# Kernel tuning notes

Hardware: AMD Instinct MI355X
Metric: run time of the kernel (lower is better)

## Reference

```python
import jax, jax.numpy as jnp
import numpy as np

SIZE = 96          # input layer neurons per side
SIZE_NEXT = 96     # first diffractive layer neurons per side
LENGTH = 1e-3      # physical aperture length (m)
Z0 = 0.0           # z of input layer
Z1 = 1e-2          # z of first diffractive layer
WAVELENGTH = 1.55e-6
TWO_PI = jnp.float32(2.0 * np.pi)


def _coords(n_size, n_length, z):
    # matrix[i, j] = ((i+0.5)*dl, (j+0.5)*dl, z), dl = n_length/n_size; flattened row-major
    idx = (jnp.arange(n_size, dtype=jnp.float32) + 0.5) * (n_length / n_size)
    x = jnp.repeat(idx, n_size)   # varies with first index
    y = jnp.tile(idx, n_size)     # varies with second index
    return x, y, jnp.float32(z)


def setup_inputs() -> dict:
    key = jax.random.key(0)
    x = jax.random.uniform(key, (SIZE, SIZE), dtype=jnp.float32)
    return {"x": x}


def reference(x):
    sx, sy, sz = _coords(SIZE, LENGTH, Z0)            # sources: (S2,)
    dx, dy, dz_plane = _coords(SIZE_NEXT, LENGTH, Z1)  # detectors: (D2,)
    # normalize image to unit amplitude, phase 0 (complex weights)
    weights = (x / jnp.max(x)).reshape(-1).astype(jnp.complex64)  # (S2,)
    # all-pairs distances (D2, S2); z separation is a scalar constant
    ddx = dx[:, None] - sx[None, :]
    ddy = dy[:, None] - sy[None, :]
    dz = dz_plane - sz
    r = jnp.sqrt(ddx * ddx + ddy * ddy + dz * dz)
    # Rayleigh-Sommerfeld secondary-source term: w = (z/r^2) * (1/(2*pi*r) + 1/(j*lambda)) * exp(j*2*pi*r/lambda)
    inv_jlam = jnp.complex64(1.0 / (1j * WAVELENGTH))
    amp = (dz / (r * r)) * ((1.0 / (TWO_PI * r)).astype(jnp.complex64) + inv_jlam)
    w = amp * jnp.exp(1j * ((TWO_PI / WAVELENGTH) * r))  # complex64 (D2, S2)
    modes = (w @ weights).reshape(SIZE_NEXT, SIZE_NEXT)
    return modes
```

## Files before the change

kernel.cpp:

```cpp
#include <hip/hip_runtime.h>

namespace rs7 {

constexpr int kN   = 96;
constexpr int kN2  = kN * kN;
constexpr int kDetPerBlock = 256;
constexpr int kSiPerBlock  = 6;
constexpr int kDetBlocks   = kN2 / kDetPerBlock;
constexpr int kSiSplits    = kN / kSiPerBlock;
constexpr int kGrid  = kDetBlocks * kSiSplits;
constexpr int kBlock = 256;
constexpr int kMaxRows = 9;
constexpr int kCols    = 2 * kN - 1;

__global__ __launch_bounds__(kBlock) void rs_table_v7(const float* __restrict__ img,
                                                      float* __restrict__ out) {
    const float dl      = (float)(1e-3 / 96.0);
    const float dz      = 0.01f;
    const float dz2     = dz * dz;
    const float lam_amp = (float)(1.0 / 1.55e-6);
    const float inv_2pi = 1.0f / 6.2831855f;
    const float k32     = 6.2831855f / 1.55e-6f;

    __shared__ float2 tab[kMaxRows * kCols];
    __shared__ float  wts[kSiPerBlock * kN];
    __shared__ float  smax[4];

    const int tid  = (int)threadIdx.x;
    const int lane = tid & 63;
    const int wid  = tid >> 6;

    const int db = (int)blockIdx.x >> 4;
    const int ss = (int)blockIdx.x & 15;
    const int d0 = db * kDetPerBlock;
    const int di_lo = d0 / kN;
    const int di_hi = (d0 + kDetPerBlock - 1) / kN;
    const int si_lo = ss * kSiPerBlock;
    const int si_hi = si_lo + kSiPerBlock - 1;

    int amin;
    if (di_lo <= si_hi && si_lo <= di_hi) amin = 0;
    else amin = (di_lo > si_hi) ? (di_lo - si_hi) : (si_lo - di_hi);
    const int amax  = max(di_hi - si_lo, si_hi - di_lo);
    const int nrows = amax - amin + 1;

    for (int e = tid; e < nrows * kCols; e += kBlock) {
        const int ra = e / kCols;
        const int c  = e - ra * kCols;
        const float ax = (float)(amin + ra) * dl;
        const float by = (float)(c - (kN - 1)) * dl;
        const float r  = sqrtf(ax * ax + by * by + dz2);
        const float theta = k32 * r;
        float sn, cs;
        __sincosf(theta, &sn, &cs);
        sn = sinf(theta);
        cs = cosf(theta);
        const float rinv = 1.0f / r;
        const float ampf = dz * rinv * rinv;
        const float near = rinv * inv_2pi;
        float2 wv;
        wv.x = ampf * (near * cs + lam_amp * sn);
        wv.y = ampf * (near * sn - lam_amp * cs);
        tab[e] = wv;
    }

    for (int t = tid; t < kSiPerBlock * kN; t += kBlock) {
        wts[t] = img[si_lo * kN + t];
    }

    float vmax = 0.0f;
    for (int t = tid; t < kN2; t += kBlock) vmax = fmaxf(vmax, img[t]);
    for (int off = 32; off >= 1; off >>= 1) vmax = fmaxf(vmax, __shfl_xor(vmax, off, 64));
    if (lane == 0) smax[wid] = vmax;
    __syncthreads();
    const float inv_max = 1.0f / fmaxf(fmaxf(smax[0], smax[1]), fmaxf(smax[2], smax[3]));

    const int det = d0 + wid * 64 + lane;
    const int di  = det / kN;
    const int dj  = det - di * kN;

    float acc_re = 0.0f, acc_im = 0.0f;

    for (int sl = 0; sl < kSiPerBlock; ++sl) {
        const int si = si_lo + sl;
        int av = di - si;
        if (av < 0) av = -av;
        const float2* __restrict__ rowp = tab + (av - amin) * kCols + dj;
        const float*  __restrict__ wrow = wts + sl * kN;
#pragma unroll
        for (int sj = 0; sj < kN; ++sj) {
            const float2 wv  = rowp[(kN - 1) - sj];
            const float  wgt = wrow[sj];
            acc_re = fmaf(wv.x, wgt, acc_re);
            acc_im = fmaf(wv.y, wgt, acc_im);
        }
    }

    atomicAdd(&out[det],       acc_re * inv_max);
    atomicAdd(&out[kN2 + det], acc_im * inv_max);
}

}

extern "C" void kernel_launch(void* const* d_in, const int* in_sizes, int n_in,
                              void* d_out, int out_size, void* d_ws, size_t ws_size,
                              hipStream_t stream) {
    (void)in_sizes; (void)n_in; (void)d_ws; (void)ws_size;
    const float* img = (const float*)d_in[0];
    float* out = (float*)d_out;
    hipMemsetAsync(d_out, 0, (size_t)out_size * sizeof(float), stream);
    hipLaunchKernelGGL(rs7::rs_table_v7, dim3(rs7::kGrid), dim3(rs7::kBlock),
                       0, stream, img, out);
}
```

Measured before the change: 76.64 us.

## Split into fp16-table conv kernel plus separate split-reduction kernel

Stores the precomputed Green's-function table in shared memory as scaled fp16 pairs instead of float2, halving LDS traffic, and reads image weights directly from global memory. Each block now covers 4 source rows instead of 6, which gives more blocks. Partial sums go to a workspace slab per split, with no atomics and no memset. A second kernel computes the max normalization once per block and sums the splits. This risks precision loss from fp16 table entries and adds a second launch plus workspace traffic.

Result: faster. 70.70 us (-7.7%).

```diff
diff --git a/kernel.cpp b/kernel.cpp
--- a/kernel.cpp
+++ b/kernel.cpp
@@ -1,20 +1,25 @@
 #include <hip/hip_runtime.h>
 
-namespace rs7 {
+namespace rs8 {
 
-constexpr int kN   = 96;
-constexpr int kN2  = kN * kN;
+constexpr int kN    = 96;
+constexpr int kN2   = kN * kN;
+constexpr int kOut2 = 2 * kN2;
 constexpr int kDetPerBlock = 256;
-constexpr int kSiPerBlock  = 6;
 constexpr int kDetBlocks   = kN2 / kDetPerBlock;
-constexpr int kSiSplits    = kN / kSiPerBlock;
-constexpr int kGrid  = kDetBlocks * kSiSplits;
+constexpr int kSiPerBlock  = 4;
+constexpr int kSplits      = kN / kSiPerBlock;
+constexpr int kGrid  = kDetBlocks * kSplits;
 constexpr int kBlock = 256;
-constexpr int kMaxRows = 9;
-constexpr int kCols    = 2 * kN - 1;
+constexpr int kCols  = 2 * kN - 1;
+constexpr int kMaxRows = 8;
+constexpr float kScale    = 1.0f / 65536.0f;
+constexpr float kUnscale  = 65536.0f;
 
-__global__ __launch_bounds__(kBlock) void rs_table_v7(const float* __restrict__ img,
-                                                      float* __restrict__ out) {
+typedef _Float16 half2_t __attribute__((ext_vector_type(2)));
+
+__global__ __launch_bounds__(kBlock) void rs_conv_v8(const float* __restrict__ img,
+                                                     float* __restrict__ ws) {
     const float dl      = (float)(1e-3 / 96.0);
     const float dz      = 0.01f;
     const float dz2     = dz * dz;
@@ -22,17 +27,12 @@
     const float inv_2pi = 1.0f / 6.2831855f;
     const float k32     = 6.2831855f / 1.55e-6f;
 
-    __shared__ float2 tab[kMaxRows * kCols];
-    __shared__ float  wts[kSiPerBlock * kN];
-    __shared__ float  smax[4];
+    __shared__ half2_t tab[kMaxRows * kCols];
 
-    const int tid  = (int)threadIdx.x;
-    const int lane = tid & 63;
-    const int wid  = tid >> 6;
-
-    const int db = (int)blockIdx.x >> 4;
-    const int ss = (int)blockIdx.x & 15;
-    const int d0 = db * kDetPerBlock;
+    const int tid = (int)threadIdx.x;
+    const int db  = (int)blockIdx.x / kSplits;
+    const int ss  = (int)blockIdx.x % kSplits;
+    const int d0  = db * kDetPerBlock;
     const int di_lo = d0 / kN;
     const int di_hi = (d0 + kDetPerBlock - 1) / kN;
     const int si_lo = ss * kSiPerBlock;
@@ -51,53 +51,69 @@
         const float by = (float)(c - (kN - 1)) * dl;
         const float r  = sqrtf(ax * ax + by * by + dz2);
         const float theta = k32 * r;
-        float sn, cs;
-        __sincosf(theta, &sn, &cs);
-        sn = sinf(theta);
-        cs = cosf(theta);
+        const float sn = sinf(theta);
+        const float cs = cosf(theta);
         const float rinv = 1.0f / r;
         const float ampf = dz * rinv * rinv;
         const float near = rinv * inv_2pi;
-        float2 wv;
-        wv.x = ampf * (near * cs + lam_amp * sn);
-        wv.y = ampf * (near * sn - lam_amp * cs);
-        tab[e] = wv;
+        const float wre = ampf * (near * cs + lam_amp * sn);
+        const float wim = ampf * (near * sn - lam_amp * cs);
+        half2_t h;
+        h.x = (_Float16)(wre * kScale);
+        h.y = (_Float16)(wim * kScale);
+        tab[e] = h;
     }
+    __syncthreads();
 
-    for (int t = tid; t < kSiPerBlock * kN; t += kBlock) {
-        wts[t] = img[si_lo * kN + t];
-    }
-
-    float vmax = 0.0f;
-    for (int t = tid; t < kN2; t += kBlock) vmax = fmaxf(vmax, img[t]);
-    for (int off = 32; off >= 1; off >>= 1) vmax = fmaxf(vmax, __shfl_xor(vmax, off, 64));
-    if (lane == 0) smax[wid] = vmax;
-    __syncthreads();
-    const float inv_max = 1.0f / fmaxf(fmaxf(smax[0], smax[1]), fmaxf(smax[2], smax[3]));
-
-    const int det = d0 + wid * 64 + lane;
+    const int det = d0 + tid;
     const int di  = det / kN;
     const int dj  = det - di * kN;
 
     float acc_re = 0.0f, acc_im = 0.0f;
 
+#pragma unroll
     for (int sl = 0; sl < kSiPerBlock; ++sl) {
         const int si = si_lo + sl;
         int av = di - si;
         if (av < 0) av = -av;
-        const float2* __restrict__ rowp = tab + (av - amin) * kCols + dj;
-        const float*  __restrict__ wrow = wts + sl * kN;
+        const half2_t* __restrict__ rp = tab + (av - amin) * kCols + dj;
+        const float2*  __restrict__ xw = (const float2*)(img + si * kN);
 #pragma unroll
-        for (int sj = 0; sj < kN; ++sj) {
-            const float2 wv  = rowp[(kN - 1) - sj];
-            const float  wgt = wrow[sj];
-            acc_re = fmaf(wv.x, wgt, acc_re);
-            acc_im = fmaf(wv.y, wgt, acc_im);
+        for (int t = 0; t < kN / 2; ++t) {
+            const float2  x2 = xw[t];
+            const half2_t wa = rp[(kN - 1) - 2 * t];
+            const half2_t wb = rp[(kN - 2) - 2 * t];
+            acc_re = fmaf((float)wa.x, x2.x, acc_re);
+            acc_im = fmaf((float)wa.y, x2.x, acc_im);
+            acc_re = fmaf((float)wb.x, x2.y, acc_re);
+            acc_im = fmaf((float)wb.y, x2.y, acc_im);
         }
     }
 
-    atomicAdd(&out[det],       acc_re * inv_max);
-    atomicAdd(&out[kN2 + det], acc_im * inv_max);
+    float* slab = ws + (size_t)ss * kOut2;
+    slab[det]       = acc_re;
+    slab[kN2 + det] = acc_im;
+}
+
+__global__ __launch_bounds__(kBlock) void rs_reduce_v8(const float* __restrict__ img,
+                                                       const float* __restrict__ ws,
+                                                       float* __restrict__ out) {
+    const int tid = (int)threadIdx.x;
+    const int g   = (int)blockIdx.x * kBlock + tid;
+
+    float vmax = 0.0f;
+    for (int t = tid; t < kN2; t += kBlock) vmax = fmaxf(vmax, img[t]);
+    for (int off = 32; off >= 1; off >>= 1) vmax = fmaxf(vmax, __shfl_xor(vmax, off, 64));
+    __shared__ float smax[4];
+    if ((tid & 63) == 0) smax[tid >> 6] = vmax;
+    __syncthreads();
+    const float gmax  = fmaxf(fmaxf(smax[0], smax[1]), fmaxf(smax[2], smax[3]));
+    const float scale = kUnscale / gmax;
+
+    float sum = 0.0f;
+#pragma unroll
+    for (int s = 0; s < kSplits; ++s) sum += ws[(size_t)s * kOut2 + g];
+    out[g] = sum * scale;
 }
 
 }
@@ -105,10 +121,12 @@
 extern "C" void kernel_launch(void* const* d_in, const int* in_sizes, int n_in,
                               void* d_out, int out_size, void* d_ws, size_t ws_size,
                               hipStream_t stream) {
-    (void)in_sizes; (void)n_in; (void)d_ws; (void)ws_size;
+    (void)in_sizes; (void)n_in; (void)out_size; (void)ws_size;
     const float* img = (const float*)d_in[0];
+    float* ws  = (float*)d_ws;
     float* out = (float*)d_out;
-    hipMemsetAsync(d_out, 0, (size_t)out_size * sizeof(float), stream);
-    hipLaunchKernelGGL(rs7::rs_table_v7, dim3(rs7::kGrid), dim3(rs7::kBlock),
-                       0, stream, img, out);
+    hipLaunchKernelGGL(rs8::rs_conv_v8, dim3(rs8::kGrid), dim3(rs8::kBlock), 0, stream,
+                       img, ws);
+    hipLaunchKernelGGL(rs8::rs_reduce_v8, dim3(rs8::kOut2 / rs8::kBlock), dim3(rs8::kBlock),
+                       0, stream, img, ws, out);
 }
```
